# Kernel tuning notes

Measured on AMD Instinct MI355X. Metric: run time of the kernel, lower is better.

## Reference

```python
import jax, jax.numpy as jnp
import numpy as np

B, S, D, E, K, DFF = 4, 2048, 1024, 8, 2, 2048  # d_ffn = 4*D//K rounded to block_size=128 -> 2048


def setup_inputs() -> dict:
    key = jax.random.key(0)
    k1, k2, k3, k4 = jax.random.split(key, 4)
    x = jax.random.normal(k1, (B, S, D), dtype=jnp.float32)
    # router: nn.Linear(D, E, bias=False) -> weight applied as x @ W^T; store as [D, E]
    router_w = jax.random.normal(k2, (D, E), dtype=jnp.float32) * 0.02
    # trunc_normal(std=0.02, a=-0.06, b=0.06) ~ clipped normal
    w1 = jnp.clip(jax.random.normal(k3, (D, DFF * E), dtype=jnp.float32) * 0.02, -0.06, 0.06)
    w2 = jnp.clip(jax.random.normal(k4, (DFF * E, D), dtype=jnp.float32) * 0.02, -0.06, 0.06)
    return {"x": x, "router_w": router_w, "w1": w1, "w2": w2}


def reference(x, router_w, w1, w2):
    b, s, d = x.shape
    x_flat = x.reshape(-1, d)                      # [T, D]
    T = x_flat.shape[0]

    # --- routing (softmax in fp32, top-k, renormalize) ---
    router_logits = x_flat @ router_w              # [T, E]
    probs = jax.nn.softmax(router_logits.astype(jnp.float32), axis=-1)
    rw, sel = jax.lax.top_k(probs, K)              # [T, K]
    rw = rw / jnp.sum(rw, axis=-1, keepdims=True)  # norm_topk_prob=True
    rw = rw.astype(x.dtype)

    # dense gate matrix [T, E]: top-k weight where selected, else 0
    gates = jnp.zeros((T, E), dtype=x.dtype).at[jnp.arange(T)[:, None], sel].add(rw)

    # --- grouped expert FFN (equivalent to sort/pad + block-sparse SDD/GELU/DSD) ---
    # w1[:, e*DFF:(e+1)*DFF] and w2[e*DFF:(e+1)*DFF, :] are expert e's weights.
    out = jnp.zeros((T, d), dtype=x.dtype)
    for e in range(E):                             # small fixed loop over experts
        h = jax.nn.gelu(x_flat @ w1[:, e * DFF:(e + 1) * DFF], approximate=False)
        out = out + gates[:, e:e + 1] * (h @ w2[e * DFF:(e + 1) * DFF, :])

    return out.reshape(b, s, d)
```

## Files before the change

### kernel.cpp

```cpp
#include <hip/hip_runtime.h>
#include <hip/hip_bf16.h>

#define T_TOK 8192
#define D_DIM 1024
#define E_NUM 8
#define TOPK 2
#define DFF_DIM 2048
#define BM 128
#define BK 64
#define MAX_TILES 136
#define MAX_PAIRS_PAD (MAX_TILES*BM)

typedef __attribute__((ext_vector_type(8))) short short8_t;
typedef __attribute__((ext_vector_type(4))) float f32x4;

__device__ __forceinline__ unsigned short f2b(float f) {
  union { float f; unsigned u; } v; v.f = f;
  unsigned u = v.u;
  return (unsigned short)((u + 0x7fffu + ((u >> 16) & 1u)) >> 16);
}

__device__ __forceinline__ float fast_gelu(float v) {
  float x = v * 0.70710678118654752f;
  float ax = fabsf(x);
  float t = __frcp_rn(1.f + 0.3275911f * ax);
  float poly = t * (0.254829592f + t * (-0.284496736f + t * (1.421413741f +
               t * (-1.453152027f + t * 1.061405429f))));
  float erfax = 1.f - poly * __expf(-x * x);
  float erfx = copysignf(erfax, x);
  return 0.5f * v * (1.f + erfx);
}

__device__ __forceinline__ void gload_lds16(const void* g, void* l) {
  __builtin_amdgcn_global_load_lds(
      (const __attribute__((address_space(1))) unsigned int*)g,
      (__attribute__((address_space(3))) unsigned int*)l, 16, 0, 0);
}

__global__ void tcvt64_kernel(const float* __restrict__ w1, unsigned short* __restrict__ w1t,
                              const float* __restrict__ w2, unsigned short* __restrict__ w2t) {
  __shared__ float tile[64][68];
  int id = blockIdx.x;
  const float* src; unsigned short* dst; int R, C, bx, by;
  if (id < 4096) { src = w1; dst = w1t; R = 1024; C = 16384; bx = id & 255; by = id >> 8; }
  else { id -= 4096; src = w2; dst = w2t; R = 16384; C = 1024; bx = id & 15; by = id >> 4; }
  const int c0 = bx * 64, r0 = by * 64;
  const int t = threadIdx.x;
  #pragma unroll
  for (int i = 0; i < 4; ++i) {
    int idx = i * 256 + t;
    int row = idx >> 4, c4 = (idx & 15) * 4;
    float4 v = *(const float4*)&src[(size_t)(r0 + row) * C + c0 + c4];
    tile[row][c4] = v.x; tile[row][c4 + 1] = v.y;
    tile[row][c4 + 2] = v.z; tile[row][c4 + 3] = v.w;
  }
  __syncthreads();
  #pragma unroll
  for (int i = 0; i < 4; ++i) {
    int idx = i * 256 + t;
    int cOut = idx >> 4, r4 = (idx & 15) * 4;
    ushort4 o;
    o.x = f2b(tile[r4][cOut]);     o.y = f2b(tile[r4 + 1][cOut]);
    o.z = f2b(tile[r4 + 2][cOut]); o.w = f2b(tile[r4 + 3][cOut]);
    *(ushort4*)&dst[(size_t)(c0 + cOut) * R + r0 + r4] = o;
  }
}

__global__ void router_kernel(const float* __restrict__ x, const float* __restrict__ rw,
                              int* __restrict__ sel, float* __restrict__ selw,
                              unsigned short* __restrict__ xb) {
  int tok = (blockIdx.x * blockDim.x + threadIdx.x) >> 6;
  int lane = threadIdx.x & 63;
  if (tok >= T_TOK) return;
  const float4* xr = (const float4*)(x + (size_t)tok * D_DIM);
  ushort4* xbr = (ushort4*)(xb + (size_t)tok * D_DIM);
  float acc[E_NUM];
  #pragma unroll
  for (int e = 0; e < E_NUM; ++e) acc[e] = 0.f;
  #pragma unroll
  for (int it = 0; it < 4; ++it) {
    int i = it * 64 + lane;
    float4 v = xr[i];
    ushort4 o;
    o.x = f2b(v.x); o.y = f2b(v.y); o.z = f2b(v.z); o.w = f2b(v.w);
    xbr[i] = o;
    const float* w = rw + (size_t)i * 4 * E_NUM;
    #pragma unroll
    for (int e = 0; e < E_NUM; ++e) acc[e] += v.x * w[e];
    #pragma unroll
    for (int e = 0; e < E_NUM; ++e) acc[e] += v.y * w[E_NUM + e];
    #pragma unroll
    for (int e = 0; e < E_NUM; ++e) acc[e] += v.z * w[2 * E_NUM + e];
    #pragma unroll
    for (int e = 0; e < E_NUM; ++e) acc[e] += v.w * w[3 * E_NUM + e];
  }
  #pragma unroll
  for (int e = 0; e < E_NUM; ++e) {
    float v = acc[e];
    #pragma unroll
    for (int off = 32; off > 0; off >>= 1) v += __shfl_xor(v, off, 64);
    acc[e] = v;
  }
  if (lane == 0) {
    float mx = acc[0];
    #pragma unroll
    for (int e = 1; e < E_NUM; ++e) mx = fmaxf(mx, acc[e]);
    float p[E_NUM];
    #pragma unroll
    for (int e = 0; e < E_NUM; ++e) p[e] = __expf(acc[e] - mx);
    int i0 = 0;
    #pragma unroll
    for (int e = 1; e < E_NUM; ++e) if (p[e] > p[i0]) i0 = e;
    int i1 = (i0 == 0) ? 1 : 0;
    #pragma unroll
    for (int e = 0; e < E_NUM; ++e) if (e != i0 && p[e] > p[i1]) i1 = e;
    float w0 = p[i0], w1 = p[i1];
    float inv = 1.f / (w0 + w1);
    sel[tok * 2] = i0; selw[tok * 2] = w0 * inv;
    sel[tok * 2 + 1] = i1; selw[tok * 2 + 1] = w1 * inv;
  }
}

__global__ void count_kernel(const int* __restrict__ sel, int* __restrict__ counts) {
  __shared__ int lc[E_NUM];
  if (threadIdx.x < E_NUM) lc[threadIdx.x] = 0;
  __syncthreads();
  int t = blockIdx.x * blockDim.x + threadIdx.x;
  if (t < 2 * T_TOK) atomicAdd(&lc[sel[t]], 1);
  __syncthreads();
  if (threadIdx.x < E_NUM) atomicAdd(&counts[threadIdx.x], lc[threadIdx.x]);
}

__global__ void plan_kernel(const int* __restrict__ counts, int* __restrict__ tiles_e,
                            int* __restrict__ tiles_b, int* __restrict__ pad_off,
                            int* __restrict__ cursor, int* __restrict__ ptok,
                            float* __restrict__ pgate, unsigned short* __restrict__ zpad) {
  if (threadIdx.x == 0) {
    int b = 0, t = 0;
    for (int e = 0; e < E_NUM; ++e) {
      pad_off[e] = b;
      int nt = (counts[e] + BM - 1) >> 7;
      for (int i = 0; i < nt; ++i) { tiles_e[t] = e; tiles_b[t] = b + i * BM; ++t; }
      b += nt * BM;
    }
    for (; t < MAX_TILES; ++t) { tiles_e[t] = -1; tiles_b[t] = 0; }
  }
  for (int i = threadIdx.x; i < MAX_PAIRS_PAD; i += blockDim.x) { ptok[i] = -1; pgate[i] = 0.f; }
  for (int i = threadIdx.x; i < 64; i += blockDim.x) zpad[i] = 0;
  if (threadIdx.x < E_NUM) cursor[threadIdx.x] = 0;
}

__global__ void scatter_kernel(const int* __restrict__ sel, const float* __restrict__ selw,
                               const int* __restrict__ pad_off, int* __restrict__ cursor,
                               int* __restrict__ ptok, float* __restrict__ pgate) {
  __shared__ int lc[E_NUM];
  __shared__ int lbase[E_NUM];
  if (threadIdx.x < E_NUM) lc[threadIdx.x] = 0;
  __syncthreads();
  int t = blockIdx.x * blockDim.x + threadIdx.x;
  int e0 = sel[t * 2], e1 = sel[t * 2 + 1];
  int o0 = atomicAdd(&lc[e0], 1);
  int o1 = atomicAdd(&lc[e1], 1);
  __syncthreads();
  if (threadIdx.x < E_NUM) lbase[threadIdx.x] = atomicAdd(&cursor[threadIdx.x], lc[threadIdx.x]);
  __syncthreads();
  int s0 = pad_off[e0] + lbase[e0] + o0;
  ptok[s0] = t; pgate[s0] = selw[t * 2];
  int s1 = pad_off[e1] + lbase[e1] + o1;
  ptok[s1] = t; pgate[s1] = selw[t * 2 + 1];
}

__global__ __launch_bounds__(256, 3) void gemm1_kernel(
    const unsigned short* __restrict__ xb, const unsigned short* __restrict__ w1t,
    const int* __restrict__ ptok, const int* __restrict__ tiles_e,
    const int* __restrict__ tiles_b, const unsigned short* __restrict__ zpad,
    unsigned short* __restrict__ h) {
  const int id = blockIdx.x + 16 * blockIdx.y;
  const int xcd = id & 7;
  const int j = id >> 3;
  const int tileIdx = xcd * 17 + (j >> 4);
  const int n0 = (j & 15) * 128;
  const int e = tiles_e[tileIdx];
  if (e < 0) return;
  const int base = tiles_b[tileIdx];

  __shared__ unsigned short As[BM * BK];
  __shared__ unsigned short Bs[BM * BK];

  const int tid = threadIdx.x;
  const int lane = tid & 63;
  const int wv = tid >> 6;
  const int wr = wv >> 1, wc = wv & 1;
  const int lr = lane & 15;
  const int lq = lane >> 4;
  const int lsw = lr & 7;

  int atok[4], aoff[4];
  const unsigned short* bptr[4];
  #pragma unroll
  for (int i = 0; i < 4; ++i) {
    int c = i * 256 + tid;
    int row = c >> 3, kc = c & 7;
    int kcs = kc ^ (row & 7);
    atok[i] = ptok[base + row];
    aoff[i] = kcs * 8;
    bptr[i] = w1t + (size_t)(e * DFF_DIM + n0 + row) * D_DIM + kcs * 8;
  }

  f32x4 acc[4][4];
  #pragma unroll
  for (int m = 0; m < 4; ++m)
    #pragma unroll
    for (int n = 0; n < 4; ++n) acc[m][n] = (f32x4){0.f, 0.f, 0.f, 0.f};

  for (int k0 = 0; k0 < D_DIM; k0 += BK) {
    #pragma unroll
    for (int i = 0; i < 4; ++i) {
      const unsigned short* ga =
          (atok[i] >= 0) ? (xb + (size_t)atok[i] * D_DIM + k0 + aoff[i]) : zpad;
      gload_lds16(ga, &As[(i * 256 + tid) * 8]);
      gload_lds16(bptr[i] + k0, &Bs[(i * 256 + tid) * 8]);
    }
    __syncthreads();
    #pragma unroll
    for (int kk = 0; kk < BK; kk += 32) {
      const int ch = (((kk >> 5) * 4 + lq) ^ lsw) * 8;
      short8_t aF[4], bF[4];
      #pragma unroll
      for (int m = 0; m < 4; ++m)
        aF[m] = *(const short8_t*)&As[(wr * 64 + m * 16 + lr) * BK + ch];
      #pragma unroll
      for (int n = 0; n < 4; ++n)
        bF[n] = *(const short8_t*)&Bs[(wc * 64 + n * 16 + lr) * BK + ch];
      #pragma unroll
      for (int m = 0; m < 4; ++m)
        #pragma unroll
        for (int n = 0; n < 4; ++n)
          acc[m][n] = __builtin_amdgcn_mfma_f32_16x16x32_bf16(aF[m], bF[n], acc[m][n], 0, 0, 0);
    }
    __syncthreads();
  }

  #pragma unroll
  for (int m = 0; m < 4; ++m) {
    #pragma unroll
    for (int n = 0; n < 4; ++n) {
      const int col = n0 + wc * 64 + n * 16 + lr;
      #pragma unroll
      for (int j4 = 0; j4 < 4; ++j4) {
        const int row = base + wr * 64 + m * 16 + lq * 4 + j4;
        h[(size_t)row * DFF_DIM + col] = f2b(fast_gelu(acc[m][n][j4]));
      }
    }
  }
}

__global__ __launch_bounds__(256, 3) void gemm2_kernel(
    const unsigned short* __restrict__ h, const unsigned short* __restrict__ w2t,
    const int* __restrict__ ptok, const float* __restrict__ pgate,
    const int* __restrict__ tiles_e, const int* __restrict__ tiles_b,
    float* __restrict__ out) {
  const int id = blockIdx.x + 8 * blockIdx.y;
  const int xcd = id & 7;
  const int j = id >> 3;
  const int tileIdx = xcd * 17 + (j >> 3);
  const int n0 = (j & 7) * 128;
  const int e = tiles_e[tileIdx];
  if (e < 0) return;
  const int base = tiles_b[tileIdx];

  __shared__ unsigned short As[BM * BK];
  __shared__ unsigned short Bs[BM * BK];

  const int tid = threadIdx.x;
  const int lane = tid & 63;
  const int wv = tid >> 6;
  const int wr = wv >> 1, wc = wv & 1;
  const int lr = lane & 15;
  const int lq = lane >> 4;
  const int lsw = lr & 7;

  const unsigned short* aptr[4];
  const unsigned short* bptr[4];
  #pragma unroll
  for (int i = 0; i < 4; ++i) {
    int c = i * 256 + tid;
    int row = c >> 3, kc = c & 7;
    int kcs = kc ^ (row & 7);
    aptr[i] = h + (size_t)(base + row) * DFF_DIM + kcs * 8;
    bptr[i] = w2t + (size_t)(n0 + row) * (E_NUM * DFF_DIM) + e * DFF_DIM + kcs * 8;
  }

  f32x4 acc[4][4];
  #pragma unroll
  for (int m = 0; m < 4; ++m)
    #pragma unroll
    for (int n = 0; n < 4; ++n) acc[m][n] = (f32x4){0.f, 0.f, 0.f, 0.f};

  for (int k0 = 0; k0 < DFF_DIM; k0 += BK) {
    #pragma unroll
    for (int i = 0; i < 4; ++i) {
      gload_lds16(aptr[i] + k0, &As[(i * 256 + tid) * 8]);
      gload_lds16(bptr[i] + k0, &Bs[(i * 256 + tid) * 8]);
    }
    __syncthreads();
    #pragma unroll
    for (int kk = 0; kk < BK; kk += 32) {
      const int ch = (((kk >> 5) * 4 + lq) ^ lsw) * 8;
      short8_t aF[4], bF[4];
      #pragma unroll
      for (int m = 0; m < 4; ++m)
        aF[m] = *(const short8_t*)&As[(wr * 64 + m * 16 + lr) * BK + ch];
      #pragma unroll
      for (int n = 0; n < 4; ++n)
        bF[n] = *(const short8_t*)&Bs[(wc * 64 + n * 16 + lr) * BK + ch];
      #pragma unroll
      for (int m = 0; m < 4; ++m)
        #pragma unroll
        for (int n = 0; n < 4; ++n)
          acc[m][n] = __builtin_amdgcn_mfma_f32_16x16x32_bf16(aF[m], bF[n], acc[m][n], 0, 0, 0);
    }
    __syncthreads();
  }

  #pragma unroll
  for (int m = 0; m < 4; ++m) {
    #pragma unroll
    for (int j4 = 0; j4 < 4; ++j4) {
      const int p = base + wr * 64 + m * 16 + lq * 4 + j4;
      const int tok = ptok[p];
      if (tok < 0) continue;
      const float g = pgate[p];
      #pragma unroll
      for (int n = 0; n < 4; ++n) {
        const int col = n0 + wc * 64 + n * 16 + lr;
        atomicAdd(&out[(size_t)tok * D_DIM + col], g * acc[m][n][j4]);
      }
    }
  }
}

extern "C" void kernel_launch(void* const* d_in, const int* in_sizes, int n_in,
                              void* d_out, int out_size, void* d_ws, size_t ws_size,
                              hipStream_t stream) {
  const float* x  = (const float*)d_in[0];
  const float* rw = (const float*)d_in[1];
  const float* w1 = (const float*)d_in[2];
  const float* w2 = (const float*)d_in[3];
  float* out = (float*)d_out;

  char* ws = (char*)d_ws;
  unsigned short* xb   = (unsigned short*)(ws);
  unsigned short* w1t  = (unsigned short*)(ws + 16777216);
  unsigned short* w2t  = (unsigned short*)(ws + 50331648);
  unsigned short* h    = (unsigned short*)(ws + 83886080);
  int*   ptok   = (int*)(ws + 155189248);
  float* pgate  = (float*)(ws + 155258880);
  int*   sel    = (int*)(ws + 155328512);
  float* selw   = (float*)(ws + 155394048);
  int*   counts = (int*)(ws + 155459584);
  int*   cursor = counts + 8;
  int*   padoff = counts + 16;
  int*   tiles_e = counts + 24;
  int*   tiles_b = tiles_e + MAX_TILES;
  unsigned short* zpad = (unsigned short*)(tiles_b + MAX_TILES);
  const size_t WS_NEED = 155459584 + 4096;
  if (ws_size < WS_NEED) return;

  hipMemsetAsync(out, 0, (size_t)T_TOK * D_DIM * sizeof(float), stream);
  hipMemsetAsync(counts, 0, E_NUM * sizeof(int), stream);

  tcvt64_kernel<<<8192, 256, 0, stream>>>(w1, w1t, w2, w2t);
  router_kernel<<<T_TOK / 4, 256, 0, stream>>>(x, rw, sel, selw, xb);
  count_kernel<<<2 * T_TOK / 256, 256, 0, stream>>>(sel, counts);
  plan_kernel<<<1, 256, 0, stream>>>(counts, tiles_e, tiles_b, padoff, cursor, ptok, pgate, zpad);
  scatter_kernel<<<T_TOK / 256, 256, 0, stream>>>(sel, selw, padoff, cursor, ptok, pgate);
  gemm1_kernel<<<dim3(DFF_DIM / 128, MAX_TILES), 256, 0, stream>>>(xb, w1t, ptok, tiles_e,
                                                                   tiles_b, zpad, h);
  gemm2_kernel<<<dim3(D_DIM / 128, MAX_TILES), 256, 0, stream>>>(h, w2t, ptok, pgate, tiles_e,
                                                                 tiles_b, out);
}
```

Measured before the change: 315.6 us.

## Double-buffer LDS tiles in both expert GEMMs to overlap loads with MFMA

Both grouped GEMM kernels now keep two LDS stages for the A and B tiles. The next k-slice is issued by direct global-to-LDS loads before the MFMA work on the current slice, and each iteration ends with one vmcnt wait plus a barrier instead of two __syncthreads. The goal is to hide global memory latency behind compute. In exchange, LDS use doubles to 64 KB per block and the launch-bounds occupancy hint drops from 3 to 2 blocks per CU.

```diff
diff --git a/kernel.cpp b/kernel.cpp
--- a/kernel.cpp
+++ b/kernel.cpp
@@ -170,7 +170,7 @@
   ptok[s1] = t; pgate[s1] = selw[t * 2 + 1];
 }
 
-__global__ __launch_bounds__(256, 3) void gemm1_kernel(
+__global__ __launch_bounds__(256, 2) void gemm1_kernel(
     const unsigned short* __restrict__ xb, const unsigned short* __restrict__ w1t,
     const int* __restrict__ ptok, const int* __restrict__ tiles_e,
     const int* __restrict__ tiles_b, const unsigned short* __restrict__ zpad,
@@ -184,8 +184,8 @@
   if (e < 0) return;
   const int base = tiles_b[tileIdx];
 
-  __shared__ unsigned short As[BM * BK];
-  __shared__ unsigned short Bs[BM * BK];
+  __shared__ unsigned short As[2][BM * BK];
+  __shared__ unsigned short Bs[2][BM * BK];
 
   const int tid = threadIdx.x;
   const int lane = tid & 63;
@@ -195,7 +195,7 @@
   const int lq = lane >> 4;
   const int lsw = lr & 7;
 
-  int atok[4], aoff[4];
+  int atok[4], aoff[4], ldst[4];
   const unsigned short* bptr[4];
   #pragma unroll
   for (int i = 0; i < 4; ++i) {
@@ -204,42 +204,52 @@
     int kcs = kc ^ (row & 7);
     atok[i] = ptok[base + row];
     aoff[i] = kcs * 8;
+    ldst[i] = c * 8;
     bptr[i] = w1t + (size_t)(e * DFF_DIM + n0 + row) * D_DIM + kcs * 8;
   }
 
+#define STAGE1(k0v, b) do {                                                        \
+    _Pragma("unroll") for (int i = 0; i < 4; ++i) {                                \
+      const unsigned short* ga =                                                   \
+          (atok[i] >= 0) ? (xb + (size_t)atok[i] * D_DIM + (k0v) + aoff[i]) : zpad;\
+      gload_lds16(ga, &As[b][ldst[i]]);                                            \
+      gload_lds16(bptr[i] + (k0v), &Bs[b][ldst[i]]);                               \
+    } } while (0)
+
   f32x4 acc[4][4];
   #pragma unroll
   for (int m = 0; m < 4; ++m)
     #pragma unroll
     for (int n = 0; n < 4; ++n) acc[m][n] = (f32x4){0.f, 0.f, 0.f, 0.f};
 
-  for (int k0 = 0; k0 < D_DIM; k0 += BK) {
-    #pragma unroll
-    for (int i = 0; i < 4; ++i) {
-      const unsigned short* ga =
-          (atok[i] >= 0) ? (xb + (size_t)atok[i] * D_DIM + k0 + aoff[i]) : zpad;
-      gload_lds16(ga, &As[(i * 256 + tid) * 8]);
-      gload_lds16(bptr[i] + k0, &Bs[(i * 256 + tid) * 8]);
-    }
-    __syncthreads();
+  STAGE1(0, 0);
+  asm volatile("s_waitcnt vmcnt(0)" ::: "memory");
+  asm volatile("s_barrier" ::: "memory");
+
+  const int NK = D_DIM / BK;
+  for (int k = 0; k < NK; ++k) {
+    const int cur = k & 1;
+    if (k + 1 < NK) STAGE1((k + 1) * BK, cur ^ 1);
     #pragma unroll
     for (int kk = 0; kk < BK; kk += 32) {
       const int ch = (((kk >> 5) * 4 + lq) ^ lsw) * 8;
       short8_t aF[4], bF[4];
       #pragma unroll
       for (int m = 0; m < 4; ++m)
-        aF[m] = *(const short8_t*)&As[(wr * 64 + m * 16 + lr) * BK + ch];
+        aF[m] = *(const short8_t*)&As[cur][(wr * 64 + m * 16 + lr) * BK + ch];
       #pragma unroll
       for (int n = 0; n < 4; ++n)
-        bF[n] = *(const short8_t*)&Bs[(wc * 64 + n * 16 + lr) * BK + ch];
+        bF[n] = *(const short8_t*)&Bs[cur][(wc * 64 + n * 16 + lr) * BK + ch];
       #pragma unroll
       for (int m = 0; m < 4; ++m)
         #pragma unroll
         for (int n = 0; n < 4; ++n)
           acc[m][n] = __builtin_amdgcn_mfma_f32_16x16x32_bf16(aF[m], bF[n], acc[m][n], 0, 0, 0);
     }
-    __syncthreads();
-  }
+    asm volatile("s_waitcnt vmcnt(0)" ::: "memory");
+    asm volatile("s_barrier" ::: "memory");
+  }
+#undef STAGE1
 
   #pragma unroll
   for (int m = 0; m < 4; ++m) {
@@ -255,7 +265,7 @@
   }
 }
 
-__global__ __launch_bounds__(256, 3) void gemm2_kernel(
+__global__ __launch_bounds__(256, 2) void gemm2_kernel(
     const unsigned short* __restrict__ h, const unsigned short* __restrict__ w2t,
     const int* __restrict__ ptok, const float* __restrict__ pgate,
     const int* __restrict__ tiles_e, const int* __restrict__ tiles_b,
@@ -269,8 +279,8 @@
   if (e < 0) return;
   const int base = tiles_b[tileIdx];
 
-  __shared__ unsigned short As[BM * BK];
-  __shared__ unsigned short Bs[BM * BK];
+  __shared__ unsigned short As[2][BM * BK];
+  __shared__ unsigned short Bs[2][BM * BK];
 
   const int tid = threadIdx.x;
   const int lane = tid & 63;
@@ -282,6 +292,7 @@
 
   const unsigned short* aptr[4];
   const unsigned short* bptr[4];
+  int ldst[4];
   #pragma unroll
   for (int i = 0; i < 4; ++i) {
     int c = i * 256 + tid;
@@ -289,7 +300,14 @@
     int kcs = kc ^ (row & 7);
     aptr[i] = h + (size_t)(base + row) * DFF_DIM + kcs * 8;
     bptr[i] = w2t + (size_t)(n0 + row) * (E_NUM * DFF_DIM) + e * DFF_DIM + kcs * 8;
-  }
+    ldst[i] = c * 8;
+  }
+
+#define STAGE2(k0v, b) do {                                                        \
+    _Pragma("unroll") for (int i = 0; i < 4; ++i) {                                \
+      gload_lds16(aptr[i] + (k0v), &As[b][ldst[i]]);                               \
+      gload_lds16(bptr[i] + (k0v), &Bs[b][ldst[i]]);                               \
+    } } while (0)
 
   f32x4 acc[4][4];
   #pragma unroll
@@ -297,31 +315,34 @@
     #pragma unroll
     for (int n = 0; n < 4; ++n) acc[m][n] = (f32x4){0.f, 0.f, 0.f, 0.f};
 
-  for (int k0 = 0; k0 < DFF_DIM; k0 += BK) {
-    #pragma unroll
-    for (int i = 0; i < 4; ++i) {
-      gload_lds16(aptr[i] + k0, &As[(i * 256 + tid) * 8]);
-      gload_lds16(bptr[i] + k0, &Bs[(i * 256 + tid) * 8]);
-    }
-    __syncthreads();
+  STAGE2(0, 0);
+  asm volatile("s_waitcnt vmcnt(0)" ::: "memory");
+  asm volatile("s_barrier" ::: "memory");
+
+  const int NK = DFF_DIM / BK;
+  for (int k = 0; k < NK; ++k) {
+    const int cur = k & 1;
+    if (k + 1 < NK) STAGE2((k + 1) * BK, cur ^ 1);
     #pragma unroll
     for (int kk = 0; kk < BK; kk += 32) {
       const int ch = (((kk >> 5) * 4 + lq) ^ lsw) * 8;
       short8_t aF[4], bF[4];
       #pragma unroll
       for (int m = 0; m < 4; ++m)
-        aF[m] = *(const short8_t*)&As[(wr * 64 + m * 16 + lr) * BK + ch];
+        aF[m] = *(const short8_t*)&As[cur][(wr * 64 + m * 16 + lr) * BK + ch];
       #pragma unroll
       for (int n = 0; n < 4; ++n)
-        bF[n] = *(const short8_t*)&Bs[(wc * 64 + n * 16 + lr) * BK + ch];
+        bF[n] = *(const short8_t*)&Bs[cur][(wc * 64 + n * 16 + lr) * BK + ch];
       #pragma unroll
       for (int m = 0; m < 4; ++m)
         #pragma unroll
         for (int n = 0; n < 4; ++n)
           acc[m][n] = __builtin_amdgcn_mfma_f32_16x16x32_bf16(aF[m], bF[n], acc[m][n], 0, 0, 0);
     }
-    __syncthreads();
-  }
+    asm volatile("s_waitcnt vmcnt(0)" ::: "memory");
+    asm volatile("s_barrier" ::: "memory");
+  }
+#undef STAGE2
 
   #pragma unroll
   for (int m = 0; m < 4; ++m) {
```

Measured after the change: 363.7 us. 1.15x slower.
